# Kernel optimization log

Hardware: AMD Instinct MI355X
Metric: run time of the kernel (lower is better)

## Reference

```python
import jax, jax.numpy as jnp
import numpy as np

B, N, C = 8, 1025, 768  # batch, tokens (1 CLS + 32*32 patches), channels
H = 12                  # heads
D = C // H              # head dim = 64
EPS = 1e-6

def _rot(x):
    # stack([-x[..., 1::2], x[..., ::2]], -1).reshape(x.shape)
    return jnp.stack([-x[..., 1::2], x[..., ::2]], axis=-1).reshape(x.shape)

def apply_rot_embed_cat(x, emb):
    # emb: [N-1, 2*D] = concat(sin, cos); x: [B, H, N-1, D]
    sin, cos = jnp.split(emb, 2, axis=-1)
    return x * cos + _rot(x) * sin

def setup_inputs() -> dict:
    key = jax.random.key(0)
    ks = jax.random.split(key, 8)
    s = 0.02
    return {
        "x": jax.random.normal(ks[0], (B, N, C), jnp.float32),
        "rope": jax.random.normal(ks[1], (N - 1, 2 * D), jnp.float32),
        "w_qkv": jax.random.normal(ks[2], (C, 3 * C), jnp.float32) * s,
        "q_bias": jax.random.normal(ks[3], (C,), jnp.float32) * s,
        "v_bias": jax.random.normal(ks[4], (C,), jnp.float32) * s,
        "gamma": jnp.ones((C,), jnp.float32),
        "beta": jnp.zeros((C,), jnp.float32),
        "w_proj": jax.random.normal(ks[5], (C, C), jnp.float32) * s,
        "b_proj": jnp.zeros((C,), jnp.float32),
    }

def reference(x, rope, w_qkv, q_bias, v_bias, gamma, beta, w_proj, b_proj):
    scale = D ** (-0.5)
    qkv_bias = jnp.concatenate([q_bias, jnp.zeros_like(q_bias), v_bias], axis=0)
    qkv = x @ w_qkv + qkv_bias  # [B, N, 3C]
    qkv = qkv.reshape(B, N, 3, H, D).transpose(2, 0, 3, 1, 4)  # [3, B, H, N, D]
    q, k, v = qkv[0], qkv[1], qkv[2]
    # RoPE on non-CLS tokens only
    q = jnp.concatenate([q[:, :, :1], apply_rot_embed_cat(q[:, :, 1:], rope)], axis=2)
    k = jnp.concatenate([k[:, :, :1], apply_rot_embed_cat(k[:, :, 1:], rope)], axis=2)
    attn = jnp.einsum('bhqd,bhkd->bhqk', q * scale, k)
    attn = jax.nn.softmax(attn, axis=-1)
    y = jnp.einsum('bhqk,bhkd->bhqd', attn, v)
    y = y.transpose(0, 2, 1, 3).reshape(B, N, C)
    # LayerNorm
    mu = jnp.mean(y, axis=-1, keepdims=True)
    var = jnp.mean(jnp.square(y - mu), axis=-1, keepdims=True)
    y = (y - mu) * jax.lax.rsqrt(var + EPS) * gamma + beta
    return y @ w_proj + b_proj
```

## Files before the change

kernel.cpp:

```cpp
#include <hip/hip_runtime.h>

typedef __bf16 bf16_t;
typedef __bf16 bf16x8 __attribute__((ext_vector_type(8)));
typedef float f32x4 __attribute__((ext_vector_type(4)));
typedef float f32x16 __attribute__((ext_vector_type(16)));
typedef unsigned short u16;
typedef unsigned int u32;

#define NTOK 1025
#define MTOT 8200
#define MPAD 8448
#define CDIM 768

__device__ __forceinline__ u16 f2bf(float f) {
  union { float f; unsigned u; } v; v.f = f;
  unsigned r = v.u + 0x7fffu + ((v.u >> 16) & 1u);
  return (u16)(r >> 16);
}
__device__ __forceinline__ float bf2f(u16 h) {
  union { unsigned u; float f; } v; v.u = ((unsigned)h) << 16; return v.f;
}
__device__ __forceinline__ u32 cvtpk(float lo, float hi) {
  u32 r; asm("v_cvt_pk_bf16_f32 %0, %1, %2" : "=v"(r) : "v"(lo), "v"(hi)); return r;
}

__global__ __launch_bounds__(256) void conv_xf(const float4* __restrict__ x4,
                                               u16* __restrict__ xf) {
  __shared__ u16 tile[16][776];
  int mt = blockIdx.x;
  int t = threadIdx.x;
#pragma unroll
  for (int it = 0; it < 12; ++it) {
    int id = it * 256 + t;
    int r = id / 192, c4 = id % 192;
    int m = mt * 16 + r;
    if (m < MTOT) {
      float4 f = x4[(size_t)m * 192 + c4];
      ushort4 o; o.x = f2bf(f.x); o.y = f2bf(f.y); o.z = f2bf(f.z); o.w = f2bf(f.w);
      *(ushort4*)&tile[r][c4 * 4] = o;
    }
  }
  __syncthreads();
#pragma unroll
  for (int it = 0; it < 6; ++it) {
    int cid = it * 256 + t;
    int kt = cid >> 6, lane = cid & 63;
    uint4 w = *(const uint4*)&tile[lane & 15][kt * 32 + (lane >> 4) * 8];
    *(uint4*)&xf[(((size_t)mt * 24 + kt) * 64 + lane) * 8] = w;
  }
}

__global__ __launch_bounds__(64) void transp_wf(const float* __restrict__ in, int N,
                                                u16* __restrict__ wf) {
  __shared__ u16 lds[16][32];
  int n0 = blockIdx.x * 16, k0 = blockIdx.y * 32;
  int t = threadIdx.x;
#pragma unroll
  for (int it = 0; it < 8; ++it) {
    int e = it * 64 + t;
    int kk = e >> 4, nn = e & 15;
    lds[nn][kk] = f2bf(in[(size_t)(k0 + kk) * N + n0 + nn]);
  }
  __syncthreads();
  uint4 w = *(const uint4*)&lds[t & 15][(t >> 4) * 8];
  *(uint4*)&wf[((((size_t)(n0 >> 4)) * 24 + (k0 >> 5)) * 64 + t) * 8] = w;
}

template <bool TRANS>
__device__ __forceinline__ void fdloop(const u16* __restrict__ afr, const u16* __restrict__ bfr,
                                       int m0, int n0, int lane, int wr, int wc,
                                       f32x4 (*acc)[4]) {
  const u16* ab = afr + ((size_t)((m0 >> 4) + wr * 4) * 24 * 64 + lane) * 8;
  const u16* bb = bfr + ((size_t)((n0 >> 4) + wc * 4) * 24 * 64 + lane) * 8;
  bf16x8 S0[8], S1[8];
  auto LOAD = [&](bf16x8 (&S)[8], int kt) {
#pragma unroll
    for (int i = 0; i < 4; ++i) S[i]     = *(const bf16x8*)(ab + (size_t)i * 12288 + kt * 512);
#pragma unroll
    for (int j = 0; j < 4; ++j) S[4 + j] = *(const bf16x8*)(bb + (size_t)j * 12288 + kt * 512);
  };
  auto COMP = [&](bf16x8 (&S)[8]) {
    __builtin_amdgcn_s_setprio(1);
#pragma unroll
    for (int x = 0; x < 4; ++x)
#pragma unroll
      for (int y = 0; y < 4; ++y)
        acc[x][y] = TRANS
            ? __builtin_amdgcn_mfma_f32_16x16x32_bf16(S[4 + x], S[y], acc[x][y], 0, 0, 0)
            : __builtin_amdgcn_mfma_f32_16x16x32_bf16(S[x], S[4 + y], acc[x][y], 0, 0, 0);
    __builtin_amdgcn_s_setprio(0);
  };
  LOAD(S0, 0);
#pragma unroll 1
  for (int k2 = 0; k2 < 11; ++k2) {
    LOAD(S1, 2 * k2 + 1);
    COMP(S0);
    LOAD(S0, 2 * k2 + 2);
    COMP(S1);
  }
  LOAD(S1, 23);
  COMP(S0);
  COMP(S1);
}

__global__ __launch_bounds__(256, 2) void qkv_gemm_t(
    const u16* __restrict__ xf, const u16* __restrict__ wf,
    const float* __restrict__ qbias, const float* __restrict__ rope,
    u16* __restrict__ q, u16* __restrict__ kfr) {
  const int NB = 12;
  int tau0 = blockIdx.x;
  int xcd = tau0 & 7, pos = tau0 >> 3;
  int tau = (xcd < 4) ? xcd * 98 + pos : 392 + (xcd - 4) * 97 + pos;
  int bx = tau % NB, by = tau / NB;
  int m0 = by * 128, n0 = bx * 128;
  int t = threadIdx.x;
  int lane = t & 63, wave = t >> 6;
  int ln = lane & 15, hi = lane >> 4;
  int wr = wave >> 1, wc = wave & 1;

  f32x4 acc[4][4] = {};
  fdloop<true>(xf, wf, m0, n0, lane, wr, wc, acc);

  const float scale = 0.125f * 1.4426950408889634f;
#pragma unroll
  for (int ii = 0; ii < 4; ++ii) {
    int m = m0 + wr * 64 + ii * 16 + ln;
    if (m < MTOT) {
      int b = m / NTOK;
      int n = m - b * NTOK;
      const float* rp = rope + (size_t)(n - 1) * 128;
#pragma unroll
      for (int jj = 0; jj < 4; ++jj) {
        int c4 = n0 + wc * 64 + jj * 16 + hi * 4;
        int part = (c4 >= CDIM) ? 1 : 0;
        int cc = c4 - part * CDIM;
        int h = cc >> 6, d4 = cc & 63;
        float v0 = acc[jj][ii][0], v1 = acc[jj][ii][1];
        float v2 = acc[jj][ii][2], v3 = acc[jj][ii][3];
        if (part == 0) {
          float4 qb = *(const float4*)(qbias + cc);
          v0 += qb.x; v1 += qb.y; v2 += qb.z; v3 += qb.w;
        }
        float o0, o1, o2, o3;
        if (n > 0) {
          float4 sn = *(const float4*)(rp + d4);
          float4 cs = *(const float4*)(rp + 64 + d4);
          o0 = v0 * cs.x - v1 * sn.x;
          o1 = v1 * cs.y + v0 * sn.y;
          o2 = v2 * cs.z - v3 * sn.z;
          o3 = v3 * cs.w + v2 * sn.w;
        } else { o0 = v0; o1 = v1; o2 = v2; o3 = v3; }
        uint2 w;
        if (part == 0) {
          w.x = cvtpk(o0 * scale, o1 * scale); w.y = cvtpk(o2 * scale, o3 * scale);
          *(uint2*)(q + ((size_t)(h * MPAD + m)) * 64 + d4) = w;
        } else {
          w.x = cvtpk(o0, o1); w.y = cvtpk(o2, o3);
          int kt2 = n >> 5, lqn = n & 31;
          int sF = d4 >> 4, h2d = (d4 >> 3) & 1, j0 = d4 & 7;
          u16* dst = kfr + ((((size_t)(h * 8 + b) * 34 + kt2) * 4 + sF) * 64
                            + h2d * 32 + lqn) * 8 + j0;
          *(uint2*)dst = w;
        }
      }
    }
  }
}

__global__ __launch_bounds__(256, 2) void qkv_gemm_v(
    const u16* __restrict__ xf, const u16* __restrict__ wf,
    const float* __restrict__ vbias, u16* __restrict__ vfr) {
  const int NB = 6;
  int tau0 = blockIdx.x;
  int xcd = tau0 & 7, pos = tau0 >> 3;
  int tau = (xcd < 6) ? xcd * 49 + pos : 294 + (xcd - 6) * 48 + pos;
  int bx = tau % NB, by = tau / NB;
  int m0 = by * 128, n0 = 1536 + bx * 128;
  int t = threadIdx.x;
  int lane = t & 63, wave = t >> 6;
  int ln = lane & 15, hi = lane >> 4;
  int wr = wave >> 1, wc = wave & 1;

  f32x4 acc[4][4] = {};
  fdloop<false>(xf, wf, m0, n0, lane, wr, wc, acc);

#pragma unroll
  for (int i = 0; i < 4; ++i) {
    int mrow = m0 + wr * 64 + i * 16 + hi * 4;
#pragma unroll
    for (int j = 0; j < 4; ++j) {
      int cv = n0 - 1536 + wc * 64 + j * 16 + ln;
      int h = cv >> 6, d = cv & 63;
      int hf = d >> 5, lqd = d & 31;
      float vb = vbias[cv];
#pragma unroll
      for (int r = 0; r < 4; ++r) {
        int mr = mrow + r;
        if (mr < MTOT) {
          int b = mr / NTOK;
          int n = mr - b * NTOK;
          size_t idx = ((((size_t)(h * 8 + b) * 17 + (n >> 6)) * 4 + ((n >> 4) & 3)) * 2 + hf) * 512
                     + (size_t)((((n >> 3) & 1) * 32 + lqd) * 8 + (n & 7));
          vfr[idx] = f2bf(acc[i][j][r] + vb);
        }
      }
    }
  }
}

template <bool PF, bool MASK>
__device__ __forceinline__ void flash_iter(
    bf16x8 (&kf)[8], bf16x8 (&kn)[8], int pftile, int it,
    const u16* kfb, const u16* vfb, int h2,
    const bf16x8 (&qf)[4], f32x16 (&acc)[2], float& l) {
  if (PF) {
    const u16* kp2 = kfb + (size_t)pftile * 4096;
#pragma unroll
    for (int c = 0; c < 2; ++c)
#pragma unroll
      for (int s = 0; s < 4; ++s)
        kn[c * 4 + s] = *(const bf16x8*)(kp2 + c * 2048 + s * 512);
  }
  bf16x8 vf[8];
  const u16* vp2 = vfb + (size_t)it * 4096;
#pragma unroll
  for (int hf = 0; hf < 2; ++hf)
#pragma unroll
    for (int s = 0; s < 4; ++s)
      vf[hf * 4 + s] = *(const bf16x8*)(vp2 + (s * 2 + hf) * 512);
  f32x16 sc[2] = {};
  __builtin_amdgcn_s_setprio(1);
#pragma unroll
  for (int c = 0; c < 2; ++c)
#pragma unroll
    for (int s = 0; s < 4; ++s)
      sc[c] = __builtin_amdgcn_mfma_f32_32x32x16_bf16(kf[c * 4 + s], qf[s], sc[c], 0, 0, 0);
  __builtin_amdgcn_s_setprio(0);
#pragma unroll
  for (int c = 0; c < 2; ++c)
#pragma unroll
    for (int r = 0; r < 16; ++r)
      sc[c][r] = __builtin_amdgcn_exp2f(sc[c][r]);
  if (MASK) {
#pragma unroll
    for (int c = 0; c < 2; ++c)
#pragma unroll
      for (int r = 0; r < 16; ++r) {
        int kk = it * 64 + c * 32 + (r & 3) + 8 * (r >> 2) + 4 * h2;
        if (kk >= NTOK) sc[c][r] = 0.f;
      }
  }
  float rs = 0.f;
#pragma unroll
  for (int c = 0; c < 2; ++c)
#pragma unroll
    for (int r = 0; r < 16; ++r) rs += sc[c][r];
  l += rs;
  bf16x8 frag[4];
#pragma unroll
  for (int c = 0; c < 2; ++c) {
    u32 k0 = cvtpk(sc[c][0], sc[c][1]),   k1 = cvtpk(sc[c][2], sc[c][3]);
    u32 k2 = cvtpk(sc[c][4], sc[c][5]),   k3 = cvtpk(sc[c][6], sc[c][7]);
    u32 k4 = cvtpk(sc[c][8], sc[c][9]),   k5 = cvtpk(sc[c][10], sc[c][11]);
    u32 k6 = cvtpk(sc[c][12], sc[c][13]), k7 = cvtpk(sc[c][14], sc[c][15]);
    asm("v_permlane32_swap_b32 %0, %1" : "+v"(k0), "+v"(k2));
    asm("v_permlane32_swap_b32 %0, %1" : "+v"(k1), "+v"(k3));
    asm("v_permlane32_swap_b32 %0, %1" : "+v"(k4), "+v"(k6));
    asm("v_permlane32_swap_b32 %0, %1" : "+v"(k5), "+v"(k7));
    union { u32 u[4]; bf16x8 v; } u0, u1;
    u0.u[0] = k0; u0.u[1] = k1; u0.u[2] = k2; u0.u[3] = k3;
    u1.u[0] = k4; u1.u[1] = k5; u1.u[2] = k6; u1.u[3] = k7;
    frag[c * 2] = u0.v; frag[c * 2 + 1] = u1.v;
  }
  __builtin_amdgcn_s_setprio(1);
#pragma unroll
  for (int hf = 0; hf < 2; ++hf)
#pragma unroll
    for (int s = 0; s < 4; ++s)
      acc[hf] = __builtin_amdgcn_mfma_f32_32x32x16_bf16(vf[hf * 4 + s], frag[s], acc[hf], 0, 0, 0);
  __builtin_amdgcn_s_setprio(0);
}

__global__ __launch_bounds__(256, 2) void flash_attn(
    const u16* __restrict__ q, const u16* __restrict__ kfr,
    const u16* __restrict__ vfr, u16* __restrict__ y) {
  int f = blockIdx.x;
  int xcd = f & 7, idx = f >> 3;
  int bh = xcd * 12 + idx / 9;
  int qt = idx - (idx / 9) * 9;
  int b = bh / 12, h = bh - b * 12;
  int t = threadIdx.x, lane = t & 63, w = t >> 6;
  int lq = lane & 31, h2 = lane >> 5;
  int q0 = qt * 128 + w * 32;
  if (q0 >= NTOK) return;
  int qrow = q0 + lq; if (qrow > NTOK - 1) qrow = NTOK - 1;

  const u16* qp = q + ((size_t)(h * MPAD) + (size_t)b * NTOK + qrow) * 64;
  bf16x8 qf[4];
#pragma unroll
  for (int s = 0; s < 4; ++s)
    qf[s] = *(const bf16x8*)&qp[s * 16 + h2 * 8];

  const u16* kfb = kfr + (size_t)(h * 8 + b) * 34 * 2048 + lane * 8;
  const u16* vfb = vfr + (size_t)(h * 8 + b) * 17 * 4096 + lane * 8;

  f32x16 acc[2] = {};
  float l = 0.f;

  bf16x8 ka[8], kb2[8];
#pragma unroll
  for (int c = 0; c < 2; ++c)
#pragma unroll
    for (int s = 0; s < 4; ++s)
      ka[c * 4 + s] = *(const bf16x8*)(kfb + c * 2048 + s * 512);

#pragma unroll 1
  for (int i2 = 0; i2 < 8; ++i2) {
    flash_iter<true, false>(ka, kb2, 2 * i2 + 1, 2 * i2, kfb, vfb, h2, qf, acc, l);
    flash_iter<true, false>(kb2, ka, 2 * i2 + 2, 2 * i2 + 1, kfb, vfb, h2, qf, acc, l);
  }
  flash_iter<false, true>(ka, kb2, 0, 16, kfb, vfb, h2, qf, acc, l);

  int row = q0 + lq;
  if (row < NTOK) {
    float lt = l + __shfl_xor(l, 32, 64);
    float inv = 1.f / lt;
    u16* yr = y + ((size_t)(b * NTOK + row)) * CDIM + h * 64;
#pragma unroll
    for (int hf = 0; hf < 2; ++hf)
#pragma unroll
      for (int g = 0; g < 4; ++g) {
        int d0 = hf * 32 + 8 * g + 4 * h2;
        ushort4 o;
        o.x = f2bf(acc[hf][g * 4 + 0] * inv);
        o.y = f2bf(acc[hf][g * 4 + 1] * inv);
        o.z = f2bf(acc[hf][g * 4 + 2] * inv);
        o.w = f2bf(acc[hf][g * 4 + 3] * inv);
        *(ushort4*)&yr[d0] = o;
      }
  }
}

__global__ __launch_bounds__(256) void lnorm(const u16* __restrict__ y,
                                             const float* __restrict__ gamma,
                                             const float* __restrict__ beta,
                                             u16* __restrict__ yf) {
  int row = blockIdx.x;
  const u16* yr = y + (size_t)row * CDIM;
  int t = threadIdx.x;
  float v[3];
  float s = 0.f, s2 = 0.f;
#pragma unroll
  for (int i = 0; i < 3; ++i) {
    v[i] = bf2f(yr[t + 256 * i]);
    s += v[i]; s2 += v[i] * v[i];
  }
#pragma unroll
  for (int msk = 1; msk < 64; msk <<= 1) {
    s  += __shfl_xor(s, msk, 64);
    s2 += __shfl_xor(s2, msk, 64);
  }
  __shared__ float ws[8];
  int w = t >> 6, lane = t & 63;
  if (lane == 0) { ws[w] = s; ws[4 + w] = s2; }
  __syncthreads();
  s = ws[0] + ws[1] + ws[2] + ws[3];
  s2 = ws[4] + ws[5] + ws[6] + ws[7];
  float mu = s * (1.f / 768.f);
  float var = s2 * (1.f / 768.f) - mu * mu;
  float rstd = rsqrtf(var + 1e-6f);
  if (t < 96) {
    union { uint4 u4; u16 u[8]; } iv, ov;
    iv.u4 = *(const uint4*)&yr[t * 8];
    const float* gp = gamma + t * 8;
    const float* bp = beta + t * 8;
#pragma unroll
    for (int j = 0; j < 8; ++j)
      ov.u[j] = f2bf((bf2f(iv.u[j]) - mu) * rstd * gp[j] + bp[j]);
    int kt = t >> 2, ln2 = (row & 15) + 16 * (t & 3), mt = row >> 4;
    *(uint4*)&yf[(((size_t)mt * 24 + kt) * 64 + ln2) * 8] = ov.u4;
  }
}

__global__ __launch_bounds__(256, 2) void proj_gemm(
    const u16* __restrict__ yf, const u16* __restrict__ wf,
    const float* __restrict__ bias, float* __restrict__ out) {
  const int NB = 6;
  int tau0 = blockIdx.x;
  int xcd = tau0 & 7, pos = tau0 >> 3;
  int tau = (xcd < 6) ? xcd * 49 + pos : 294 + (xcd - 6) * 48 + pos;
  int bx = tau % NB, by = tau / NB;
  int m0 = by * 128, n0 = bx * 128;
  int t = threadIdx.x;
  int lane = t & 63, wave = t >> 6;
  int ln = lane & 15, hi = lane >> 4;
  int wr = wave >> 1, wc = wave & 1;

  f32x4 acc[4][4] = {};
  fdloop<true>(yf, wf, m0, n0, lane, wr, wc, acc);

#pragma unroll
  for (int ii = 0; ii < 4; ++ii) {
    int m = m0 + wr * 64 + ii * 16 + ln;
    if (m < MTOT) {
      float* dr = out + (size_t)m * CDIM;
#pragma unroll
      for (int jj = 0; jj < 4; ++jj) {
        int c4 = n0 + wc * 64 + jj * 16 + hi * 4;
        float4 bv = *(const float4*)(bias + c4);
        float4 o;
        o.x = acc[jj][ii][0] + bv.x;
        o.y = acc[jj][ii][1] + bv.y;
        o.z = acc[jj][ii][2] + bv.z;
        o.w = acc[jj][ii][3] + bv.w;
        *(float4*)(dr + c4) = o;
      }
    }
  }
}

extern "C" void kernel_launch(void* const* d_in, const int* in_sizes, int n_in,
                              void* d_out, int out_size, void* d_ws, size_t ws_size,
                              hipStream_t stream) {
  const float* x      = (const float*)d_in[0];
  const float* rope   = (const float*)d_in[1];
  const float* w_qkv  = (const float*)d_in[2];
  const float* q_bias = (const float*)d_in[3];
  const float* v_bias = (const float*)d_in[4];
  const float* gamma  = (const float*)d_in[5];
  const float* beta   = (const float*)d_in[6];
  const float* w_proj = (const float*)d_in[7];
  const float* b_proj = (const float*)d_in[8];
  float* out = (float*)d_out;

  char* ws = (char*)d_ws;
  u16* xf   = (u16*)(ws);
  u16* ybf  = (u16*)(ws);
  u16* wfq  = (u16*)(ws + 12976128);
  u16* wfp  = (u16*)(ws + 16515072);
  u16* qbuf = (u16*)(ws + 17694720);
  u16* yf   = (u16*)(ws + 17694720);
  u16* kfr  = (u16*)(ws + 30670848);
  u16* vfr  = (u16*)(ws + 44040192);

  conv_xf<<<dim3(513), 256, 0, stream>>>((const float4*)x, xf);
  transp_wf<<<dim3(144, 24), 64, 0, stream>>>(w_qkv, 2304, wfq);
  transp_wf<<<dim3(48, 24), 64, 0, stream>>>(w_proj, 768, wfp);

  qkv_gemm_t<<<dim3(780), 256, 0, stream>>>(xf, wfq, q_bias, rope, qbuf, kfr);
  qkv_gemm_v<<<dim3(390), 256, 0, stream>>>(xf, wfq, v_bias, vfr);
  flash_attn<<<dim3(864), 256, 0, stream>>>(qbuf, kfr, vfr, ybf);
  lnorm<<<8200, 256, 0, stream>>>(ybf, gamma, beta, yf);
  proj_gemm<<<dim3(390), 256, 0, stream>>>(yf, wfp, b_proj, out);
}
```

Baseline: 167.2 us.

## Triple-buffer GEMM loads and hand-schedule flash-attention loads with explicit vmcnt waits

The fragment GEMM loop moves from double-buffered compiler-scheduled loads to a fully unrolled triple buffer. Loads are issued as inline-asm global_load_dwordx4 with explicit s_waitcnt vmcnt and sched barriers, so two k-tiles stay in flight during each MFMA block. Flash attention now issues V loads before the next K prefetch and waits only for the data each MFMA phase needs, so V latency can overlap the QK and softmax stages. The cost is more live VGPRs and reliance on hand-counted vmcnt values: the compiler does not track these asm loads, so a miscount or register reuse would break correctness.

```diff
diff --git a/kernel.cpp b/kernel.cpp
--- a/kernel.cpp
+++ b/kernel.cpp
@@ -11,6 +11,9 @@
 #define MTOT 8200
 #define MPAD 8448
 #define CDIM 768
+
+#define GLOAD(dst, p) \
+  asm volatile("global_load_dwordx4 %0, %1, off" : "=&v"(dst) : "v"((const void*)(p)))
 
 __device__ __forceinline__ u16 f2bf(float f) {
   union { float f; unsigned u; } v; v.f = f;
@@ -70,37 +73,43 @@
 __device__ __forceinline__ void fdloop(const u16* __restrict__ afr, const u16* __restrict__ bfr,
                                        int m0, int n0, int lane, int wr, int wc,
                                        f32x4 (*acc)[4]) {
-  const u16* ab = afr + ((size_t)((m0 >> 4) + wr * 4) * 24 * 64 + lane) * 8;
-  const u16* bb = bfr + ((size_t)((n0 >> 4) + wc * 4) * 24 * 64 + lane) * 8;
-  bf16x8 S0[8], S1[8];
-  auto LOAD = [&](bf16x8 (&S)[8], int kt) {
-#pragma unroll
-    for (int i = 0; i < 4; ++i) S[i]     = *(const bf16x8*)(ab + (size_t)i * 12288 + kt * 512);
-#pragma unroll
-    for (int j = 0; j < 4; ++j) S[4 + j] = *(const bf16x8*)(bb + (size_t)j * 12288 + kt * 512);
+  const u16* ab = afr + ((size_t)((m0 >> 4) + wr * 4) * 1536 + lane) * 8;
+  const u16* bb = bfr + ((size_t)((n0 >> 4) + wc * 4) * 1536 + lane) * 8;
+  bf16x8 S[3][8];
+  auto LOADA = [&](int s, int kt) {
+#pragma unroll
+    for (int i = 0; i < 4; ++i)
+      GLOAD(S[s][i], ab + (size_t)i * 12288 + (size_t)kt * 512);
+#pragma unroll
+    for (int j = 0; j < 4; ++j)
+      GLOAD(S[s][4 + j], bb + (size_t)j * 12288 + (size_t)kt * 512);
   };
-  auto COMP = [&](bf16x8 (&S)[8]) {
+  auto COMP = [&](bf16x8 (&Sc)[8]) {
     __builtin_amdgcn_s_setprio(1);
 #pragma unroll
     for (int x = 0; x < 4; ++x)
 #pragma unroll
       for (int y = 0; y < 4; ++y)
         acc[x][y] = TRANS
-            ? __builtin_amdgcn_mfma_f32_16x16x32_bf16(S[4 + x], S[y], acc[x][y], 0, 0, 0)
-            : __builtin_amdgcn_mfma_f32_16x16x32_bf16(S[x], S[4 + y], acc[x][y], 0, 0, 0);
+            ? __builtin_amdgcn_mfma_f32_16x16x32_bf16(Sc[4 + x], Sc[y], acc[x][y], 0, 0, 0)
+            : __builtin_amdgcn_mfma_f32_16x16x32_bf16(Sc[x], Sc[4 + y], acc[x][y], 0, 0, 0);
     __builtin_amdgcn_s_setprio(0);
   };
-  LOAD(S0, 0);
-#pragma unroll 1
-  for (int k2 = 0; k2 < 11; ++k2) {
-    LOAD(S1, 2 * k2 + 1);
-    COMP(S0);
-    LOAD(S0, 2 * k2 + 2);
-    COMP(S1);
-  }
-  LOAD(S1, 23);
-  COMP(S0);
-  COMP(S1);
+  LOADA(0, 0);
+  LOADA(1, 1);
+#pragma unroll
+  for (int kt = 0; kt < 24; ++kt) {
+    if (kt < 22) {
+      LOADA((kt + 2) % 3, kt + 2);
+      asm volatile("s_waitcnt vmcnt(16)");
+    } else if (kt == 22) {
+      asm volatile("s_waitcnt vmcnt(8)");
+    } else {
+      asm volatile("s_waitcnt vmcnt(0)");
+    }
+    __builtin_amdgcn_sched_barrier(0);
+    COMP(S[kt % 3]);
+  }
 }
 
 __global__ __launch_bounds__(256, 2) void qkv_gemm_t(
@@ -213,21 +222,24 @@
     bf16x8 (&kf)[8], bf16x8 (&kn)[8], int pftile, int it,
     const u16* kfb, const u16* vfb, int h2,
     const bf16x8 (&qf)[4], f32x16 (&acc)[2], float& l) {
+  bf16x8 vf[8];
+  const u16* vp2 = vfb + (size_t)it * 4096;
+#pragma unroll
+  for (int hf = 0; hf < 2; ++hf)
+#pragma unroll
+    for (int s = 0; s < 4; ++s)
+      GLOAD(vf[hf * 4 + s], vp2 + (s * 2 + hf) * 512);
   if (PF) {
     const u16* kp2 = kfb + (size_t)pftile * 4096;
 #pragma unroll
     for (int c = 0; c < 2; ++c)
 #pragma unroll
       for (int s = 0; s < 4; ++s)
-        kn[c * 4 + s] = *(const bf16x8*)(kp2 + c * 2048 + s * 512);
-  }
-  bf16x8 vf[8];
-  const u16* vp2 = vfb + (size_t)it * 4096;
-#pragma unroll
-  for (int hf = 0; hf < 2; ++hf)
-#pragma unroll
-    for (int s = 0; s < 4; ++s)
-      vf[hf * 4 + s] = *(const bf16x8*)(vp2 + (s * 2 + hf) * 512);
+        GLOAD(kn[c * 4 + s], kp2 + c * 2048 + s * 512);
+  }
+  if (PF) asm volatile("s_waitcnt vmcnt(16)");
+  else    asm volatile("s_waitcnt vmcnt(8)");
+  __builtin_amdgcn_sched_barrier(0);
   f32x16 sc[2] = {};
   __builtin_amdgcn_s_setprio(1);
 #pragma unroll
@@ -272,6 +284,9 @@
     u1.u[0] = k4; u1.u[1] = k5; u1.u[2] = k6; u1.u[3] = k7;
     frag[c * 2] = u0.v; frag[c * 2 + 1] = u1.v;
   }
+  if (PF) asm volatile("s_waitcnt vmcnt(8)");
+  else    asm volatile("s_waitcnt vmcnt(0)");
+  __builtin_amdgcn_sched_barrier(0);
   __builtin_amdgcn_s_setprio(1);
 #pragma unroll
   for (int hf = 0; hf < 2; ++hf)
@@ -312,7 +327,7 @@
   for (int c = 0; c < 2; ++c)
 #pragma unroll
     for (int s = 0; s < 4; ++s)
-      ka[c * 4 + s] = *(const bf16x8*)(kfb + c * 2048 + s * 512);
+      GLOAD(ka[c * 4 + s], kfb + c * 2048 + s * 512);
 
 #pragma unroll 1
   for (int i2 = 0; i2 < 8; ++i2) {
```

Result: slower. 171.2 us (+2.4%).
